# Kernel tuning notes

Measured on AMD Instinct MI355X. Metric: run time of the kernel, lower is better.

## Reference

```python
import jax, jax.numpy as jnp
import numpy as np

H = 8        # num_heads
D = 64       # qkv_dim
E = 512      # embed_dim = H*D
MS = 16      # ms_hidden_dim


def setup_inputs() -> dict:
    key = jax.random.key(0)
    ks = jax.random.split(key, 12)
    b, r, c = 4, 512, 512
    row_emb = jax.random.normal(ks[0], (b, r, E), dtype=jnp.float32)
    col_emb = jax.random.normal(ks[1], (b, c, E), dtype=jnp.float32)
    cost_mat = jax.random.uniform(ks[2], (b, r, c), dtype=jnp.float32)
    attn_mask = jax.random.randint(ks[3], (b, H, r, c), 0, 2) > 0
    s = 1.0 / np.sqrt(E)
    Wq = jax.random.uniform(ks[4], (H * D, E), minval=-s, maxval=s)
    Wk = jax.random.uniform(ks[5], (H * D, E), minval=-s, maxval=s)
    Wv = jax.random.uniform(ks[6], (H * D, E), minval=-s, maxval=s)
    Wout = jax.random.uniform(ks[7], (E, E), minval=-s, maxval=s)
    m1 = np.sqrt(0.5)
    m2 = np.sqrt(1.0 / MS)
    Wmix1 = jax.random.uniform(ks[8], (H * MS, 2 * H), minval=-m1, maxval=m1)
    Wmix2 = jax.random.uniform(ks[9], (H, H * MS), minval=-m2, maxval=m2)
    return {"row_emb": row_emb, "col_emb": col_emb, "cost_mat": cost_mat,
            "attn_mask": attn_mask, "Wq": Wq, "Wk": Wk, "Wv": Wv,
            "Wmix1": Wmix1, "Wmix2": Wmix2, "Wout": Wout}


def reference(row_emb, col_emb, cost_mat, attn_mask, Wq, Wk, Wv, Wmix1, Wmix2, Wout):
    b, r, _ = row_emb.shape
    c = col_emb.shape[1]
    norm = 1.0 / jnp.sqrt(jnp.asarray(D, row_emb.dtype))
    # projections -> [b, h, s, d]
    q = (row_emb @ Wq.T).reshape(b, r, H, D).transpose(0, 2, 1, 3)
    k = (col_emb @ Wk.T).reshape(b, c, H, D).transpose(0, 2, 1, 3)
    v = (col_emb @ Wv.T).reshape(b, c, H, D).transpose(0, 2, 1, 3)
    dot = norm * jnp.einsum('bhrd,bhcd->bhrc', q, k)            # [b,h,r,c]
    cost = jnp.broadcast_to(cost_mat[:, None, :, :], dot.shape)  # [b,h,r,c]
    # stack then rearrange 'b h r c s -> b r c (h s)' (h major, s minor)
    two = jnp.stack([dot, cost], axis=-1)                        # [b,h,r,c,2]
    two = two.transpose(0, 2, 3, 1, 4).reshape(b, r, c, 2 * H)
    hid = jax.nn.relu(two @ Wmix1.T)                             # [b,r,c,H*MS]
    ms = hid @ Wmix2.T                                           # [b,r,c,H]
    logits = ms.transpose(0, 3, 1, 2)                            # [b,h,r,c]
    # mask handling: rows that are fully masked become fully unmasked
    all_masked = jnp.all(attn_mask, axis=-1, keepdims=True)
    mask = jnp.where(all_masked, False, attn_mask)
    logits = jnp.where(mask, -jnp.inf, logits)
    weights = jax.nn.softmax(logits, axis=-1)
    out = jnp.einsum('bhrc,bhcd->bhrd', weights, v)              # [b,h,r,d]
    out = out.transpose(0, 2, 1, 3).reshape(b, r, H * D)         # b s (h d)
    return out @ Wout.T
```

## Files before the change

kernel.cpp:

```cpp
#include <hip/hip_runtime.h>
#include <math.h>

typedef __attribute__((ext_vector_type(8))) short bf16x8;
typedef __attribute__((ext_vector_type(4))) float f32x4;
typedef unsigned short ushort_t;

static __device__ inline unsigned short f2bf(float f) {
    union { float f; unsigned u; } v; v.f = f;
    unsigned r = v.u + 0x7fff + ((v.u >> 16) & 1);
    return (unsigned short)(r >> 16);
}

static __device__ inline unsigned pk2bf(float a, float b) {
    unsigned r;
    asm("v_cvt_pk_bf16_f32 %0, %1, %2" : "=v"(r) : "v"(a), "v"(b));
    return r;
}

__global__ __launch_bounds__(256) void convert_all(const float* __restrict__ a0,
                                                   const float* __restrict__ a1,
                                                   const float* __restrict__ a2,
                                                   const float* __restrict__ a3,
                                                   const float* __restrict__ a4,
                                                   const float* __restrict__ a5,
                                                   ushort_t* __restrict__ dst) {
    const size_t e = ((size_t)blockIdx.x * 256 + threadIdx.x) * 4;
    const float* src; size_t off;
    if      (e < 1048576) { src = a0; off = 0; }
    else if (e < 2097152) { src = a1; off = 1048576; }
    else if (e < 2359296) { src = a2; off = 2097152; }
    else if (e < 2621440) { src = a3; off = 2359296; }
    else if (e < 2883584) { src = a4; off = 2621440; }
    else                  { src = a5; off = 2883584; }
    const float4 v = *(const float4*)(src + (e - off));
    uint2 o; o.x = pk2bf(v.x, v.y); o.y = pk2bf(v.z, v.w);
    *(uint2*)(dst + e) = o;
}

__global__ __launch_bounds__(256) void gemm_qkv(const ushort_t* __restrict__ rowb,
                                                const ushort_t* __restrict__ colb,
                                                const ushort_t* __restrict__ Wqb,
                                                const ushort_t* __restrict__ Wkb,
                                                const ushort_t* __restrict__ Wvb,
                                                ushort_t* __restrict__ Qb,
                                                ushort_t* __restrict__ Kb,
                                                ushort_t* __restrict__ Vt) {
    const int z = blockIdx.z;
    const ushort_t* A = (z == 0) ? rowb : colb;
    const ushort_t* B = (z == 0) ? Wqb : (z == 1) ? Wkb : Wvb;

    const int t    = threadIdx.x;
    const int w    = t >> 6;
    const int lane = t & 63;
    const int quad = lane >> 4;
    const int sl   = lane & 15;
    const int m0 = blockIdx.x * 64 + (w >> 1) * 32;
    const int n0 = blockIdx.y * 64 + (w & 1) * 32;

    f32x4 acc[2][2] = {};

    for (int k0 = 0; k0 < 512; k0 += 32) {
        bf16x8 a[2], b[2];
#pragma unroll
        for (int rs = 0; rs < 2; ++rs)
            a[rs] = *(const bf16x8*)(A + (size_t)(m0 + rs * 16 + sl) * 512 + k0 + quad * 8);
#pragma unroll
        for (int cs = 0; cs < 2; ++cs)
            b[cs] = *(const bf16x8*)(B + (size_t)(n0 + cs * 16 + sl) * 512 + k0 + quad * 8);
#pragma unroll
        for (int rs = 0; rs < 2; ++rs)
#pragma unroll
            for (int cs = 0; cs < 2; ++cs)
                acc[rs][cs] = __builtin_amdgcn_mfma_f32_16x16x32_bf16(a[rs], b[cs], acc[rs][cs], 0, 0, 0);
    }

#pragma unroll
    for (int rs = 0; rs < 2; ++rs)
#pragma unroll
        for (int cs = 0; cs < 2; ++cs) {
            const int n = n0 + cs * 16 + sl;
            if (z == 2) {
                const int mb   = m0 + rs * 16 + quad * 4;
                const int bidx = mb >> 9, c = mb & 511;
                const int h = n >> 6, d = n & 63;
                uint2 o;
                o.x = pk2bf(acc[rs][cs][0], acc[rs][cs][1]);
                o.y = pk2bf(acc[rs][cs][2], acc[rs][cs][3]);
                *(uint2*)(Vt + (size_t)(((bidx * 8 + h) * 64 + d)) * 512 + c) = o;
            } else {
                ushort_t* C = (z == 0) ? Qb : Kb;
#pragma unroll
                for (int reg = 0; reg < 4; ++reg) {
                    const int m = m0 + rs * 16 + quad * 4 + reg;
                    C[(size_t)m * 512 + n] = f2bf(acc[rs][cs][reg]);
                }
            }
        }
}

__global__ __launch_bounds__(256) void gemm_out(const ushort_t* __restrict__ A,
                                                const ushort_t* __restrict__ B,
                                                float* __restrict__ C) {
    const int t    = threadIdx.x;
    const int w    = t >> 6;
    const int lane = t & 63;
    const int quad = lane >> 4;
    const int sl   = lane & 15;
    const int m0 = blockIdx.x * 64 + (w >> 1) * 32;
    const int n0 = blockIdx.y * 64 + (w & 1) * 32;

    f32x4 acc[2][2] = {};

    for (int k0 = 0; k0 < 512; k0 += 32) {
        bf16x8 a[2], b[2];
#pragma unroll
        for (int rs = 0; rs < 2; ++rs)
            a[rs] = *(const bf16x8*)(A + (size_t)(m0 + rs * 16 + sl) * 512 + k0 + quad * 8);
#pragma unroll
        for (int cs = 0; cs < 2; ++cs)
            b[cs] = *(const bf16x8*)(B + (size_t)(n0 + cs * 16 + sl) * 512 + k0 + quad * 8);
#pragma unroll
        for (int rs = 0; rs < 2; ++rs)
#pragma unroll
            for (int cs = 0; cs < 2; ++cs)
                acc[rs][cs] = __builtin_amdgcn_mfma_f32_16x16x32_bf16(a[rs], b[cs], acc[rs][cs], 0, 0, 0);
    }

#pragma unroll
    for (int rs = 0; rs < 2; ++rs)
#pragma unroll
        for (int cs = 0; cs < 2; ++cs) {
            const int n = n0 + cs * 16 + sl;
#pragma unroll
            for (int reg = 0; reg < 4; ++reg) {
                const int m = m0 + rs * 16 + quad * 4 + reg;
                C[(size_t)m * 512 + n] = acc[rs][cs][reg];
            }
        }
}

__global__ __launch_bounds__(256) void dot_mlp_v7(const ushort_t* __restrict__ Qb,
                                                  const ushort_t* __restrict__ Kb,
                                                  const float* __restrict__ cost,
                                                  const float* __restrict__ W1,
                                                  const float* __restrict__ W2,
                                                  float* __restrict__ logits) {
    __shared__ ushort_t Xs[512 * 20];
    __shared__ ushort_t W1fs[128 * 16];
    __shared__ ushort_t W2ss[8 * 128];

    const int b  = blockIdx.z;
    const int r0 = blockIdx.y * 32;
    const int c0 = blockIdx.x * 16;
    const int t    = threadIdx.x;
    const int w    = t >> 6;
    const int lane = t & 63;
    const int quad = lane >> 4;
    const int sl   = lane & 15;

    const bf16x8 zf = {0, 0, 0, 0, 0, 0, 0, 0};

    if (t < 128) {
        float s = 0.f;
#pragma unroll
        for (int h = 0; h < 8; ++h) {
            W1fs[t * 16 + h] = f2bf(W1[t * 16 + 2 * h]);
            s += W1[t * 16 + 2 * h + 1];
        }
        W1fs[t * 16 + 8] = f2bf(s);
#pragma unroll
        for (int k = 9; k < 16; ++k) W1fs[t * 16 + k] = 0;
    }
#pragma unroll
    for (int i = 0; i < 4; ++i) W2ss[t + i * 256] = f2bf(W2[t + i * 256]);

#pragma unroll
    for (int i = 0; i < 2; ++i) {
        const int cell = t + i * 256;
        const int rl = cell >> 4, cl = cell & 15;
        unsigned* base = (unsigned*)(Xs + cell * 20) + 4;
        base[0] = (unsigned)f2bf(cost[((size_t)b * 512 + r0 + rl) * 512 + c0 + cl]);
        base[1] = 0; base[2] = 0; base[3] = 0;
    }

    {
        const int rs  = w >> 1;
        const int hbj = w & 1;
        unsigned uu[2][4];
#pragma unroll
        for (int hp = 0; hp < 2; ++hp) {
            const int h0 = hbj * 4 + hp * 2;
            bf16x8 qa[2][2], ka[2][2];
#pragma unroll
            for (int hh = 0; hh < 2; ++hh)
#pragma unroll
                for (int ks = 0; ks < 2; ++ks) {
                    qa[hh][ks] = *(const bf16x8*)(Qb +
                        ((size_t)(b * 512 + r0 + rs * 16 + sl) * 512 + (h0 + hh) * 64 + ks * 32 + quad * 8));
                    ka[hh][ks] = *(const bf16x8*)(Kb +
                        ((size_t)(b * 512 + c0 + sl) * 512 + (h0 + hh) * 64 + ks * 32 + quad * 8));
                }
            f32x4 ac0 = {0.f, 0.f, 0.f, 0.f}, ac1 = {0.f, 0.f, 0.f, 0.f};
            ac0 = __builtin_amdgcn_mfma_f32_16x16x32_bf16(qa[0][0], ka[0][0], ac0, 0, 0, 0);
            ac0 = __builtin_amdgcn_mfma_f32_16x16x32_bf16(qa[0][1], ka[0][1], ac0, 0, 0, 0);
            ac1 = __builtin_amdgcn_mfma_f32_16x16x32_bf16(qa[1][0], ka[1][0], ac1, 0, 0, 0);
            ac1 = __builtin_amdgcn_mfma_f32_16x16x32_bf16(qa[1][1], ka[1][1], ac1, 0, 0, 0);
#pragma unroll
            for (int reg = 0; reg < 4; ++reg)
                uu[hp][reg] = pk2bf(ac0[reg] * 0.125f, ac1[reg] * 0.125f);
        }
        const int rowb = rs * 16 + quad * 4;
#pragma unroll
        for (int reg = 0; reg < 4; ++reg) {
            const int cell = (rowb + reg) * 16 + sl;
            unsigned* xp = (unsigned*)(Xs + cell * 20) + hbj * 2;
            xp[0] = uu[0][reg];
            xp[1] = uu[1][reg];
        }
    }

    __syncthreads();

    bf16x8 aw1[8];
#pragma unroll
    for (int nt = 0; nt < 8; ++nt)
        aw1[nt] = (quad < 2) ? *(const bf16x8*)&W1fs[(nt * 16 + sl) * 16 + quad * 8] : zf;

    bf16x8 w2f[4];
#pragma unroll
    for (int ks = 0; ks < 4; ++ks) {
        union { ushort_t s[8]; bf16x8 v; } tu;
#pragma unroll
        for (int i = 0; i < 8; ++i) {
            const int j = (2 * ks + (i >> 2)) * 16 + quad * 4 + (i & 3);
            tu.s[i] = (sl < 8) ? W2ss[sl * 128 + j] : (ushort_t)0;
        }
        w2f[ks] = tu.v;
    }

#pragma unroll
    for (int mt = 0; mt < 8; ++mt) {
        const int gmt  = w * 8 + mt;
        const int cell = gmt * 16 + sl;

        bf16x8 a1 = zf;
        if (quad < 2) {
            const unsigned* xr = (const unsigned*)Xs + (size_t)cell * 10 + quad * 4;
            union { unsigned u[4]; bf16x8 v; } tmp;
            tmp.u[0] = xr[0]; tmp.u[1] = xr[1]; tmp.u[2] = xr[2]; tmp.u[3] = xr[3];
            a1 = tmp.v;
        }

        f32x4 acc2 = {0.f, 0.f, 0.f, 0.f};
#pragma unroll
        for (int ks = 0; ks < 4; ++ks) {
            f32x4 z = {0.f, 0.f, 0.f, 0.f};
            const f32x4 h0v = __builtin_amdgcn_mfma_f32_16x16x32_bf16(aw1[2 * ks],     a1, z, 0, 0, 0);
            const f32x4 h1v = __builtin_amdgcn_mfma_f32_16x16x32_bf16(aw1[2 * ks + 1], a1, z, 0, 0, 0);
            union { unsigned u[4]; bf16x8 v; } hb;
            hb.u[0] = pk2bf(fmaxf(h0v[0], 0.f), fmaxf(h0v[1], 0.f));
            hb.u[1] = pk2bf(fmaxf(h0v[2], 0.f), fmaxf(h0v[3], 0.f));
            hb.u[2] = pk2bf(fmaxf(h1v[0], 0.f), fmaxf(h1v[1], 0.f));
            hb.u[3] = pk2bf(fmaxf(h1v[2], 0.f), fmaxf(h1v[3], 0.f));
            acc2 = __builtin_amdgcn_mfma_f32_16x16x32_bf16(w2f[ks], hb.v, acc2, 0, 0, 0);
        }

        if (quad < 2) {
            const int r = r0 + gmt;
            const int c = c0 + sl;
#pragma unroll
            for (int reg = 0; reg < 4; ++reg) {
                const int h = quad * 4 + reg;
                logits[((size_t)(b * 8 + h) * 512 + r) * 512 + c] = acc2[reg];
            }
        }
    }
}

__global__ __launch_bounds__(256) void softmax_pv(const float* __restrict__ logits,
                                                  const int* __restrict__ mask,
                                                  const ushort_t* __restrict__ Vt,
                                                  ushort_t* __restrict__ Aout) {
    __shared__ ushort_t Ps[32 * 522];

    const int t    = threadIdx.x;
    const int w    = t >> 6;
    const int lane = t & 63;
    const int quad = lane >> 4;
    const int sl   = lane & 15;
    const int rt = blockIdx.x;
    const int bh = blockIdx.y;
    const int r0 = rt * 32;

#pragma unroll
    for (int rr = 0; rr < 8; ++rr) {
        const int row = w * 8 + rr;
        const float* lp = logits + ((size_t)bh * 512 + r0 + row) * 512;
        const int*   mp = mask   + ((size_t)bh * 512 + r0 + row) * 512;

        const float4 f0 = ((const float4*)lp)[lane];
        const float4 f1 = ((const float4*)lp)[lane + 64];
        const int4   m0 = ((const int4*)mp)[lane];
        const int4   m1 = ((const int4*)mp)[lane + 64];

        float v[8]; int m[8];
        v[0] = f0.x; v[1] = f0.y; v[2] = f0.z; v[3] = f0.w;
        v[4] = f1.x; v[5] = f1.y; v[6] = f1.z; v[7] = f1.w;
        m[0] = m0.x; m[1] = m0.y; m[2] = m0.z; m[3] = m0.w;
        m[4] = m1.x; m[5] = m1.y; m[6] = m1.z; m[7] = m1.w;

        int allm = 1;
#pragma unroll
        for (int i = 0; i < 8; ++i) allm &= (m[i] != 0);
        const bool all_masked = (__all(allm) != 0);

        float mx = -__builtin_inff();
#pragma unroll
        for (int i = 0; i < 8; ++i) {
            const bool keep = all_masked || (m[i] == 0);
            if (keep) mx = fmaxf(mx, v[i]);
        }
#pragma unroll
        for (int s = 32; s > 0; s >>= 1) mx = fmaxf(mx, __shfl_xor(mx, s, 64));

        float e[8]; float sum = 0.f;
#pragma unroll
        for (int i = 0; i < 8; ++i) {
            const bool keep = all_masked || (m[i] == 0);
            e[i] = keep ? __expf(v[i] - mx) : 0.f;
            sum += e[i];
        }
#pragma unroll
        for (int s = 32; s > 0; s >>= 1) sum += __shfl_xor(sum, s, 64);

        const float inv = 1.f / sum;
        unsigned* pr = (unsigned*)Ps + 261 * row + 2 * lane;
        pr[0]   = pk2bf(e[0] * inv, e[1] * inv);
        pr[1]   = pk2bf(e[2] * inv, e[3] * inv);
        pr[128] = pk2bf(e[4] * inv, e[5] * inv);
        pr[129] = pk2bf(e[6] * inv, e[7] * inv);
    }

    __syncthreads();

    const int mt  = w >> 1;
    const int n0w = (w & 1) * 32;
    const ushort_t* vb = Vt + (size_t)bh * 64 * 512;

    f32x4 acc[2] = {};
#pragma unroll 4
    for (int ks = 0; ks < 16; ++ks) {
        union { unsigned u[4]; bf16x8 v; } ta;
        const ushort_t* pp = Ps + (size_t)(mt * 16 + sl) * 522 + ks * 32 + quad * 8;
        ta.u[0] = *(const unsigned*)(pp);
        ta.u[1] = *(const unsigned*)(pp + 2);
        ta.u[2] = *(const unsigned*)(pp + 4);
        ta.u[3] = *(const unsigned*)(pp + 6);
        bf16x8 bv[2];
#pragma unroll
        for (int cn = 0; cn < 2; ++cn)
            bv[cn] = *(const bf16x8*)(vb + (size_t)(n0w + cn * 16 + sl) * 512 + ks * 32 + quad * 8);
#pragma unroll
        for (int cn = 0; cn < 2; ++cn)
            acc[cn] = __builtin_amdgcn_mfma_f32_16x16x32_bf16(ta.v, bv[cn], acc[cn], 0, 0, 0);
    }

    const int bidx = bh >> 3, h = bh & 7;
    ushort_t* Cb = Aout + (size_t)bidx * 512 * 512 + h * 64;
#pragma unroll
    for (int cn = 0; cn < 2; ++cn) {
        const int n = n0w + cn * 16 + sl;
#pragma unroll
        for (int reg = 0; reg < 4; ++reg) {
            const int m = r0 + mt * 16 + quad * 4 + reg;
            Cb[(size_t)m * 512 + n] = f2bf(acc[cn][reg]);
        }
    }
}

extern "C" void kernel_launch(void* const* d_in, const int* in_sizes, int n_in,
                              void* d_out, int out_size, void* d_ws, size_t ws_size,
                              hipStream_t stream) {
    const float* row_emb = (const float*)d_in[0];
    const float* col_emb = (const float*)d_in[1];
    const float* cost    = (const float*)d_in[2];
    const int*   mask    = (const int*)d_in[3];
    const float* Wq      = (const float*)d_in[4];
    const float* Wk      = (const float*)d_in[5];
    const float* Wv      = (const float*)d_in[6];
    const float* Wmix1   = (const float*)d_in[7];
    const float* Wmix2   = (const float*)d_in[8];
    const float* Wout    = (const float*)d_in[9];
    float* out = (float*)d_out;

    char* ws = (char*)d_ws;
    const size_t MB = (size_t)1 << 20;
    ushort_t* convDst = (ushort_t*)ws;
    ushort_t* rowb  = (ushort_t*)(ws);
    ushort_t* colb  = (ushort_t*)(ws + 2 * MB);
    ushort_t* Wqb   = (ushort_t*)(ws + 4 * MB);
    ushort_t* Wkb   = (ushort_t*)(ws + 4 * MB + 512 * 1024);
    ushort_t* Wvb   = (ushort_t*)(ws + 5 * MB);
    ushort_t* Woutb = (ushort_t*)(ws + 5 * MB + 512 * 1024);
    ushort_t* Qb    = (ushort_t*)(ws + 6 * MB);
    ushort_t* Kb    = (ushort_t*)(ws + 8 * MB);
    ushort_t* Vt    = (ushort_t*)(ws + 10 * MB);
    ushort_t* Aoutb = (ushort_t*)(ws + 12 * MB);
    float* logitsBuf = (float*)(ws + 40 * MB);

    convert_all<<<3072, 256, 0, stream>>>(row_emb, col_emb, Wq, Wk, Wv, Wout, convDst);

    gemm_qkv<<<dim3(32, 8, 3), 256, 0, stream>>>(rowb, colb, Wqb, Wkb, Wvb, Qb, Kb, Vt);

    dot_mlp_v7<<<dim3(32, 16, 4), 256, 0, stream>>>(Qb, Kb, cost, Wmix1, Wmix2, logitsBuf);

    softmax_pv<<<dim3(16, 32), 256, 0, stream>>>(logitsBuf, mask, Vt, Aoutb);

    gemm_out<<<dim3(32, 8), 256, 0, stream>>>(Aoutb, Woutb, out);
}
```

Before: 178.9 us.

## Precompute mix-MLP weight fragments once and keep dot tiles in registers

```diff
diff --git a/kernel.cpp b/kernel.cpp
--- a/kernel.cpp
+++ b/kernel.cpp
@@ -23,7 +23,51 @@
                                                    const float* __restrict__ a3,
                                                    const float* __restrict__ a4,
                                                    const float* __restrict__ a5,
-                                                   ushort_t* __restrict__ dst) {
+                                                   const float* __restrict__ W1,
+                                                   const float* __restrict__ W2,
+                                                   ushort_t* __restrict__ dst,
+                                                   ushort_t* __restrict__ tab) {
+    if (blockIdx.x >= 3072) {
+        const int t = threadIdx.x;
+        if (t < 64) {
+            const int quad = t >> 4;
+            const int sl   = t & 15;
+#pragma unroll
+            for (int nt = 0; nt < 8; ++nt) {
+                union { ushort_t s[8]; uint4 u; } vv;
+#pragma unroll
+                for (int i = 0; i < 8; ++i) vv.s[i] = 0;
+                if (quad < 2) {
+                    const int j = nt * 16 + sl;
+#pragma unroll
+                    for (int i = 0; i < 8; ++i) {
+                        const int k = quad * 8 + i;
+                        if (k < 8) {
+                            vv.s[i] = f2bf(W1[j * 16 + 2 * k]);
+                        } else if (k == 8) {
+                            float s = 0.f;
+#pragma unroll
+                            for (int h = 0; h < 8; ++h) s += W1[j * 16 + 2 * h + 1];
+                            vv.s[i] = f2bf(s);
+                        }
+                    }
+                }
+                *(uint4*)(tab + (nt * 64 + t) * 8) = vv.u;
+            }
+#pragma unroll
+            for (int ks = 0; ks < 4; ++ks) {
+                union { ushort_t s[8]; uint4 u; } vv;
+#pragma unroll
+                for (int i = 0; i < 8; ++i) {
+                    const int j = (2 * ks + (i >> 2)) * 16 + quad * 4 + (i & 3);
+                    vv.s[i] = (sl < 8) ? f2bf(W2[sl * 128 + j]) : (ushort_t)0;
+                }
+                *(uint4*)(tab + 4096 + (ks * 64 + t) * 8) = vv.u;
+            }
+        }
+        return;
+    }
+
     const size_t e = ((size_t)blockIdx.x * 256 + threadIdx.x) * 4;
     const float* src; size_t off;
     if      (e < 1048576) { src = a0; off = 0; }
@@ -139,124 +183,79 @@
         }
 }
 
-__global__ __launch_bounds__(256) void dot_mlp_v7(const ushort_t* __restrict__ Qb,
+__global__ __launch_bounds__(256) void dot_mlp_v8(const ushort_t* __restrict__ Qb,
                                                   const ushort_t* __restrict__ Kb,
                                                   const float* __restrict__ cost,
-                                                  const float* __restrict__ W1,
-                                                  const float* __restrict__ W2,
+                                                  const ushort_t* __restrict__ tab,
                                                   float* __restrict__ logits) {
-    __shared__ ushort_t Xs[512 * 20];
-    __shared__ ushort_t W1fs[128 * 16];
-    __shared__ ushort_t W2ss[8 * 128];
-
     const int b  = blockIdx.z;
-    const int r0 = blockIdx.y * 32;
     const int c0 = blockIdx.x * 16;
     const int t    = threadIdx.x;
     const int w    = t >> 6;
     const int lane = t & 63;
     const int quad = lane >> 4;
     const int sl   = lane & 15;
-
-    const bf16x8 zf = {0, 0, 0, 0, 0, 0, 0, 0};
-
-    if (t < 128) {
-        float s = 0.f;
+    const int r0w  = blockIdx.y * 64 + w * 16;
+
+    unsigned pdw[4][4];
+    {
+        f32x4 acc[8];
 #pragma unroll
         for (int h = 0; h < 8; ++h) {
-            W1fs[t * 16 + h] = f2bf(W1[t * 16 + 2 * h]);
-            s += W1[t * 16 + 2 * h + 1];
-        }
-        W1fs[t * 16 + 8] = f2bf(s);
-#pragma unroll
-        for (int k = 9; k < 16; ++k) W1fs[t * 16 + k] = 0;
-    }
-#pragma unroll
-    for (int i = 0; i < 4; ++i) W2ss[t + i * 256] = f2bf(W2[t + i * 256]);
-
-#pragma unroll
-    for (int i = 0; i < 2; ++i) {
-        const int cell = t + i * 256;
-        const int rl = cell >> 4, cl = cell & 15;
-        unsigned* base = (unsigned*)(Xs + cell * 20) + 4;
-        base[0] = (unsigned)f2bf(cost[((size_t)b * 512 + r0 + rl) * 512 + c0 + cl]);
-        base[1] = 0; base[2] = 0; base[3] = 0;
-    }
-
-    {
-        const int rs  = w >> 1;
-        const int hbj = w & 1;
-        unsigned uu[2][4];
-#pragma unroll
-        for (int hp = 0; hp < 2; ++hp) {
-            const int h0 = hbj * 4 + hp * 2;
-            bf16x8 qa[2][2], ka[2][2];
-#pragma unroll
-            for (int hh = 0; hh < 2; ++hh)
-#pragma unroll
-                for (int ks = 0; ks < 2; ++ks) {
-                    qa[hh][ks] = *(const bf16x8*)(Qb +
-                        ((size_t)(b * 512 + r0 + rs * 16 + sl) * 512 + (h0 + hh) * 64 + ks * 32 + quad * 8));
-                    ka[hh][ks] = *(const bf16x8*)(Kb +
-                        ((size_t)(b * 512 + c0 + sl) * 512 + (h0 + hh) * 64 + ks * 32 + quad * 8));
-                }
-            f32x4 ac0 = {0.f, 0.f, 0.f, 0.f}, ac1 = {0.f, 0.f, 0.f, 0.f};
-            ac0 = __builtin_amdgcn_mfma_f32_16x16x32_bf16(qa[0][0], ka[0][0], ac0, 0, 0, 0);
-            ac0 = __builtin_amdgcn_mfma_f32_16x16x32_bf16(qa[0][1], ka[0][1], ac0, 0, 0, 0);
-            ac1 = __builtin_amdgcn_mfma_f32_16x16x32_bf16(qa[1][0], ka[1][0], ac1, 0, 0, 0);
-            ac1 = __builtin_amdgcn_mfma_f32_16x16x32_bf16(qa[1][1], ka[1][1], ac1, 0, 0, 0);
+            const ushort_t* qp = Qb + (size_t)(b * 512 + r0w + sl) * 512 + h * 64 + quad * 8;
+            const ushort_t* kp = Kb + (size_t)(b * 512 + c0  + sl) * 512 + h * 64 + quad * 8;
+            const bf16x8 q0 = *(const bf16x8*)(qp);
+            const bf16x8 q1 = *(const bf16x8*)(qp + 32);
+            const bf16x8 k0 = *(const bf16x8*)(kp);
+            const bf16x8 k1 = *(const bf16x8*)(kp + 32);
+            f32x4 a = {0.f, 0.f, 0.f, 0.f};
+            a = __builtin_amdgcn_mfma_f32_16x16x32_bf16(q0, k0, a, 0, 0, 0);
+            a = __builtin_amdgcn_mfma_f32_16x16x32_bf16(q1, k1, a, 0, 0, 0);
+            acc[h] = a;
+        }
+#pragma unroll
+        for (int hp = 0; hp < 4; ++hp)
 #pragma unroll
             for (int reg = 0; reg < 4; ++reg)
-                uu[hp][reg] = pk2bf(ac0[reg] * 0.125f, ac1[reg] * 0.125f);
-        }
-        const int rowb = rs * 16 + quad * 4;
-#pragma unroll
-        for (int reg = 0; reg < 4; ++reg) {
-            const int cell = (rowb + reg) * 16 + sl;
-            unsigned* xp = (unsigned*)(Xs + cell * 20) + hbj * 2;
-            xp[0] = uu[0][reg];
-            xp[1] = uu[1][reg];
-        }
-    }
-
-    __syncthreads();
-
-    bf16x8 aw1[8];
+                pdw[hp][reg] = pk2bf(acc[2 * hp][reg] * 0.125f, acc[2 * hp + 1][reg] * 0.125f);
+    }
+
+    unsigned costd[4];
+#pragma unroll
+    for (int j = 0; j < 4; ++j)
+        costd[j] = (unsigned)f2bf(cost[((size_t)(b * 512) + r0w + quad * 4 + j) * 512 + c0 + sl]);
+
+    bf16x8 aw1[8], w2f[4];
 #pragma unroll
     for (int nt = 0; nt < 8; ++nt)
-        aw1[nt] = (quad < 2) ? *(const bf16x8*)&W1fs[(nt * 16 + sl) * 16 + quad * 8] : zf;
-
-    bf16x8 w2f[4];
-#pragma unroll
-    for (int ks = 0; ks < 4; ++ks) {
-        union { ushort_t s[8]; bf16x8 v; } tu;
-#pragma unroll
-        for (int i = 0; i < 8; ++i) {
-            const int j = (2 * ks + (i >> 2)) * 16 + quad * 4 + (i & 3);
-            tu.s[i] = (sl < 8) ? W2ss[sl * 128 + j] : (ushort_t)0;
-        }
-        w2f[ks] = tu.v;
-    }
-
-#pragma unroll
-    for (int mt = 0; mt < 8; ++mt) {
-        const int gmt  = w * 8 + mt;
-        const int cell = gmt * 16 + sl;
-
-        bf16x8 a1 = zf;
-        if (quad < 2) {
-            const unsigned* xr = (const unsigned*)Xs + (size_t)cell * 10 + quad * 4;
-            union { unsigned u[4]; bf16x8 v; } tmp;
-            tmp.u[0] = xr[0]; tmp.u[1] = xr[1]; tmp.u[2] = xr[2]; tmp.u[3] = xr[3];
-            a1 = tmp.v;
-        }
+        aw1[nt] = *(const bf16x8*)(tab + (nt * 64 + lane) * 8);
+#pragma unroll
+    for (int ks = 0; ks < 4; ++ks)
+        w2f[ks] = *(const bf16x8*)(tab + 4096 + (ks * 64 + lane) * 8);
+
+#pragma unroll
+    for (int mt = 0; mt < 16; ++mt) {
+        const int qs = mt >> 2, rg = mt & 3;
+        const int ba = (qs * 16 + sl) * 4;
+
+        const unsigned rr0 = (unsigned)__builtin_amdgcn_ds_bpermute(ba, (int)pdw[0][rg]);
+        const unsigned rr1 = (unsigned)__builtin_amdgcn_ds_bpermute(ba, (int)pdw[1][rg]);
+        const unsigned rr2 = (unsigned)__builtin_amdgcn_ds_bpermute(ba, (int)pdw[2][rg]);
+        const unsigned rr3 = (unsigned)__builtin_amdgcn_ds_bpermute(ba, (int)pdw[3][rg]);
+        const unsigned rrc = (unsigned)__builtin_amdgcn_ds_bpermute(ba, (int)costd[rg]);
+
+        union { unsigned u[4]; bf16x8 v; } af;
+        af.u[0] = (quad == 0) ? rr0 : ((quad == 1) ? rrc : 0u);
+        af.u[1] = (quad == 0) ? rr1 : 0u;
+        af.u[2] = (quad == 0) ? rr2 : 0u;
+        af.u[3] = (quad == 0) ? rr3 : 0u;
 
         f32x4 acc2 = {0.f, 0.f, 0.f, 0.f};
 #pragma unroll
         for (int ks = 0; ks < 4; ++ks) {
             f32x4 z = {0.f, 0.f, 0.f, 0.f};
-            const f32x4 h0v = __builtin_amdgcn_mfma_f32_16x16x32_bf16(aw1[2 * ks],     a1, z, 0, 0, 0);
-            const f32x4 h1v = __builtin_amdgcn_mfma_f32_16x16x32_bf16(aw1[2 * ks + 1], a1, z, 0, 0, 0);
+            const f32x4 h0v = __builtin_amdgcn_mfma_f32_16x16x32_bf16(aw1[2 * ks],     af.v, z, 0, 0, 0);
+            const f32x4 h1v = __builtin_amdgcn_mfma_f32_16x16x32_bf16(aw1[2 * ks + 1], af.v, z, 0, 0, 0);
             union { unsigned u[4]; bf16x8 v; } hb;
             hb.u[0] = pk2bf(fmaxf(h0v[0], 0.f), fmaxf(h0v[1], 0.f));
             hb.u[1] = pk2bf(fmaxf(h0v[2], 0.f), fmaxf(h0v[3], 0.f));
@@ -266,12 +265,11 @@
         }
 
         if (quad < 2) {
-            const int r = r0 + gmt;
-            const int c = c0 + sl;
+            const int rG = r0w + mt;
 #pragma unroll
             for (int reg = 0; reg < 4; ++reg) {
                 const int h = quad * 4 + reg;
-                logits[((size_t)(b * 8 + h) * 512 + r) * 512 + c] = acc2[reg];
+                logits[((size_t)(b * 8 + h) * 512 + rG) * 512 + c0 + sl] = acc2[reg];
             }
         }
     }
@@ -406,13 +404,15 @@
     ushort_t* Kb    = (ushort_t*)(ws + 8 * MB);
     ushort_t* Vt    = (ushort_t*)(ws + 10 * MB);
     ushort_t* Aoutb = (ushort_t*)(ws + 12 * MB);
+    ushort_t* fragTab = (ushort_t*)(ws + 14 * MB);
     float* logitsBuf = (float*)(ws + 40 * MB);
 
-    convert_all<<<3072, 256, 0, stream>>>(row_emb, col_emb, Wq, Wk, Wv, Wout, convDst);
+    convert_all<<<3073, 256, 0, stream>>>(row_emb, col_emb, Wq, Wk, Wv, Wout,
+                                          Wmix1, Wmix2, convDst, fragTab);
 
     gemm_qkv<<<dim3(32, 8, 3), 256, 0, stream>>>(rowb, colb, Wqb, Wkb, Wvb, Qb, Kb, Vt);
 
-    dot_mlp_v7<<<dim3(32, 16, 4), 256, 0, stream>>>(Qb, Kb, cost, Wmix1, Wmix2, logitsBuf);
+    dot_mlp_v8<<<dim3(32, 8, 4), 256, 0, stream>>>(Qb, Kb, cost, fragTab, logitsBuf);
 
     softmax_pv<<<dim3(16, 32), 256, 0, stream>>>(logitsBuf, mask, Vt, Aoutb);
 
```

Result: slower. 188.8 us (+5.5%).

## Store logits as fp16 and precompute mixer MFMA fragments in convert kernel

Applied to the files above, without the earlier changes.

```diff
diff --git a/kernel.cpp b/kernel.cpp
--- a/kernel.cpp
+++ b/kernel.cpp
@@ -3,6 +3,7 @@
 
 typedef __attribute__((ext_vector_type(8))) short bf16x8;
 typedef __attribute__((ext_vector_type(4))) float f32x4;
+typedef __attribute__((ext_vector_type(8))) _Float16 f16x8_t;
 typedef unsigned short ushort_t;
 
 static __device__ inline unsigned short f2bf(float f) {
@@ -23,7 +24,51 @@
                                                    const float* __restrict__ a3,
                                                    const float* __restrict__ a4,
                                                    const float* __restrict__ a5,
-                                                   ushort_t* __restrict__ dst) {
+                                                   const float* __restrict__ W1,
+                                                   const float* __restrict__ W2,
+                                                   ushort_t* __restrict__ dst,
+                                                   ushort_t* __restrict__ tab) {
+    if (blockIdx.x >= 3072) {
+        const int t = threadIdx.x;
+        if (t < 64) {
+            const int quad = t >> 4;
+            const int sl   = t & 15;
+#pragma unroll
+            for (int nt = 0; nt < 8; ++nt) {
+                union { ushort_t s[8]; uint4 u; } vv;
+#pragma unroll
+                for (int i = 0; i < 8; ++i) vv.s[i] = 0;
+                if (quad < 2) {
+                    const int j = nt * 16 + sl;
+#pragma unroll
+                    for (int i = 0; i < 8; ++i) {
+                        const int k = quad * 8 + i;
+                        if (k < 8) {
+                            vv.s[i] = f2bf(W1[j * 16 + 2 * k]);
+                        } else if (k == 8) {
+                            float s = 0.f;
+#pragma unroll
+                            for (int h = 0; h < 8; ++h) s += W1[j * 16 + 2 * h + 1];
+                            vv.s[i] = f2bf(s);
+                        }
+                    }
+                }
+                *(uint4*)(tab + (nt * 64 + t) * 8) = vv.u;
+            }
+#pragma unroll
+            for (int ks = 0; ks < 4; ++ks) {
+                union { ushort_t s[8]; uint4 u; } vv;
+#pragma unroll
+                for (int i = 0; i < 8; ++i) {
+                    const int j = (2 * ks + (i >> 2)) * 16 + quad * 4 + (i & 3);
+                    vv.s[i] = (sl < 8) ? f2bf(W2[sl * 128 + j]) : (ushort_t)0;
+                }
+                *(uint4*)(tab + 4096 + (ks * 64 + t) * 8) = vv.u;
+            }
+        }
+        return;
+    }
+
     const size_t e = ((size_t)blockIdx.x * 256 + threadIdx.x) * 4;
     const float* src; size_t off;
     if      (e < 1048576) { src = a0; off = 0; }
@@ -139,15 +184,12 @@
         }
 }
 
-__global__ __launch_bounds__(256) void dot_mlp_v7(const ushort_t* __restrict__ Qb,
+__global__ __launch_bounds__(256) void dot_mlp_v9(const ushort_t* __restrict__ Qb,
                                                   const ushort_t* __restrict__ Kb,
                                                   const float* __restrict__ cost,
-                                                  const float* __restrict__ W1,
-                                                  const float* __restrict__ W2,
-                                                  float* __restrict__ logits) {
+                                                  const ushort_t* __restrict__ tab,
+                                                  _Float16* __restrict__ logits) {
     __shared__ ushort_t Xs[512 * 20];
-    __shared__ ushort_t W1fs[128 * 16];
-    __shared__ ushort_t W2ss[8 * 128];
 
     const int b  = blockIdx.z;
     const int r0 = blockIdx.y * 32;
@@ -158,22 +200,6 @@
     const int quad = lane >> 4;
     const int sl   = lane & 15;
 
-    const bf16x8 zf = {0, 0, 0, 0, 0, 0, 0, 0};
-
-    if (t < 128) {
-        float s = 0.f;
-#pragma unroll
-        for (int h = 0; h < 8; ++h) {
-            W1fs[t * 16 + h] = f2bf(W1[t * 16 + 2 * h]);
-            s += W1[t * 16 + 2 * h + 1];
-        }
-        W1fs[t * 16 + 8] = f2bf(s);
-#pragma unroll
-        for (int k = 9; k < 16; ++k) W1fs[t * 16 + k] = 0;
-    }
-#pragma unroll
-    for (int i = 0; i < 4; ++i) W2ss[t + i * 256] = f2bf(W2[t + i * 256]);
-
 #pragma unroll
     for (int i = 0; i < 2; ++i) {
         const int cell = t + i * 256;
@@ -182,6 +208,14 @@
         base[0] = (unsigned)f2bf(cost[((size_t)b * 512 + r0 + rl) * 512 + c0 + cl]);
         base[1] = 0; base[2] = 0; base[3] = 0;
     }
+
+    bf16x8 aw1[8], w2f[4];
+#pragma unroll
+    for (int nt = 0; nt < 8; ++nt)
+        aw1[nt] = *(const bf16x8*)(tab + (nt * 64 + lane) * 8);
+#pragma unroll
+    for (int ks = 0; ks < 4; ++ks)
+        w2f[ks] = *(const bf16x8*)(tab + 4096 + (ks * 64 + lane) * 8);
 
     {
         const int rs  = w >> 1;
@@ -221,23 +255,7 @@
 
     __syncthreads();
 
-    bf16x8 aw1[8];
-#pragma unroll
-    for (int nt = 0; nt < 8; ++nt)
-        aw1[nt] = (quad < 2) ? *(const bf16x8*)&W1fs[(nt * 16 + sl) * 16 + quad * 8] : zf;
-
-    bf16x8 w2f[4];
-#pragma unroll
-    for (int ks = 0; ks < 4; ++ks) {
-        union { ushort_t s[8]; bf16x8 v; } tu;
-#pragma unroll
-        for (int i = 0; i < 8; ++i) {
-            const int j = (2 * ks + (i >> 2)) * 16 + quad * 4 + (i & 3);
-            tu.s[i] = (sl < 8) ? W2ss[sl * 128 + j] : (ushort_t)0;
-        }
-        w2f[ks] = tu.v;
-    }
-
+    const bf16x8 zf = {0, 0, 0, 0, 0, 0, 0, 0};
 #pragma unroll
     for (int mt = 0; mt < 8; ++mt) {
         const int gmt  = w * 8 + mt;
@@ -271,13 +289,13 @@
 #pragma unroll
             for (int reg = 0; reg < 4; ++reg) {
                 const int h = quad * 4 + reg;
-                logits[((size_t)(b * 8 + h) * 512 + r) * 512 + c] = acc2[reg];
+                logits[((size_t)(b * 8 + h) * 512 + r) * 512 + c] = (_Float16)acc2[reg];
             }
         }
     }
 }
 
-__global__ __launch_bounds__(256) void softmax_pv(const float* __restrict__ logits,
+__global__ __launch_bounds__(256) void softmax_pv(const _Float16* __restrict__ logits,
                                                   const int* __restrict__ mask,
                                                   const ushort_t* __restrict__ Vt,
                                                   ushort_t* __restrict__ Aout) {
@@ -295,17 +313,16 @@
 #pragma unroll
     for (int rr = 0; rr < 8; ++rr) {
         const int row = w * 8 + rr;
-        const float* lp = logits + ((size_t)bh * 512 + r0 + row) * 512;
-        const int*   mp = mask   + ((size_t)bh * 512 + r0 + row) * 512;
-
-        const float4 f0 = ((const float4*)lp)[lane];
-        const float4 f1 = ((const float4*)lp)[lane + 64];
-        const int4   m0 = ((const int4*)mp)[lane];
-        const int4   m1 = ((const int4*)mp)[lane + 64];
+        const _Float16* lp = logits + ((size_t)bh * 512 + r0 + row) * 512;
+        const int*      mp = mask   + ((size_t)bh * 512 + r0 + row) * 512;
+
+        const f16x8_t fv = ((const f16x8_t*)lp)[lane];
+        const int4    m0 = ((const int4*)mp)[2 * lane];
+        const int4    m1 = ((const int4*)mp)[2 * lane + 1];
 
         float v[8]; int m[8];
-        v[0] = f0.x; v[1] = f0.y; v[2] = f0.z; v[3] = f0.w;
-        v[4] = f1.x; v[5] = f1.y; v[6] = f1.z; v[7] = f1.w;
+#pragma unroll
+        for (int i = 0; i < 8; ++i) v[i] = (float)fv[i];
         m[0] = m0.x; m[1] = m0.y; m[2] = m0.z; m[3] = m0.w;
         m[4] = m1.x; m[5] = m1.y; m[6] = m1.z; m[7] = m1.w;
 
@@ -334,11 +351,11 @@
         for (int s = 32; s > 0; s >>= 1) sum += __shfl_xor(sum, s, 64);
 
         const float inv = 1.f / sum;
-        unsigned* pr = (unsigned*)Ps + 261 * row + 2 * lane;
-        pr[0]   = pk2bf(e[0] * inv, e[1] * inv);
-        pr[1]   = pk2bf(e[2] * inv, e[3] * inv);
-        pr[128] = pk2bf(e[4] * inv, e[5] * inv);
-        pr[129] = pk2bf(e[6] * inv, e[7] * inv);
+        unsigned* pr = (unsigned*)Ps + 261 * row + 4 * lane;
+        pr[0] = pk2bf(e[0] * inv, e[1] * inv);
+        pr[1] = pk2bf(e[2] * inv, e[3] * inv);
+        pr[2] = pk2bf(e[4] * inv, e[5] * inv);
+        pr[3] = pk2bf(e[6] * inv, e[7] * inv);
     }
 
     __syncthreads();
@@ -406,13 +423,15 @@
     ushort_t* Kb    = (ushort_t*)(ws + 8 * MB);
     ushort_t* Vt    = (ushort_t*)(ws + 10 * MB);
     ushort_t* Aoutb = (ushort_t*)(ws + 12 * MB);
-    float* logitsBuf = (float*)(ws + 40 * MB);
-
-    convert_all<<<3072, 256, 0, stream>>>(row_emb, col_emb, Wq, Wk, Wv, Wout, convDst);
+    ushort_t* fragTab = (ushort_t*)(ws + 14 * MB);
+    _Float16* logitsBuf = (_Float16*)(ws + 40 * MB);
+
+    convert_all<<<3073, 256, 0, stream>>>(row_emb, col_emb, Wq, Wk, Wv, Wout,
+                                          Wmix1, Wmix2, convDst, fragTab);
 
     gemm_qkv<<<dim3(32, 8, 3), 256, 0, stream>>>(rowb, colb, Wqb, Wkb, Wvb, Qb, Kb, Vt);
 
-    dot_mlp_v7<<<dim3(32, 16, 4), 256, 0, stream>>>(Qb, Kb, cost, Wmix1, Wmix2, logitsBuf);
+    dot_mlp_v9<<<dim3(32, 16, 4), 256, 0, stream>>>(Qb, Kb, cost, fragTab, logitsBuf);
 
     softmax_pv<<<dim3(16, 32), 256, 0, stream>>>(logitsBuf, mask, Vt, Aoutb);
 
```

Measured after the change: 186.4 us. 1.04x slower.
